# Kernel tuning notes

Measured on AMD Instinct MI355X. Metric: run time of the kernel, lower is better.

## Reference

```python
import jax, jax.numpy as jnp
import numpy as np

EPS = 1e-6

def _ln(x):
    m = jnp.mean(x, -1, keepdims=True)
    v = jnp.mean((x - m) ** 2, -1, keepdims=True)
    return (x - m) * jax.lax.rsqrt(v + EPS)

def _rms(x, w):
    return x * jax.lax.rsqrt(jnp.mean(x * x, -1, keepdims=True) + EPS) * w

def _rotate_half(x):
    xr = x.reshape(x.shape[:-1] + (-1, 2))
    return jnp.stack([-xr[..., 1], xr[..., 0]], axis=-1).reshape(x.shape)

def _rope(x, cos, sin):
    # x: [B,L,H,D]; cos/sin: [L,D] interleaved-duplicated per pair
    c = cos[None, :, None, :]
    s = sin[None, :, None, :]
    return x * c + _rotate_half(x) * s

def _modulate(x, shift, scale):
    return x * (1.0 + scale[:, None, :]) + shift[:, None, :]

def _gate(x, g):
    return x * g[:, None, :]

def setup_inputs() -> dict:
    key = jax.random.key(0)
    ks = jax.random.split(key, 20)
    B, LI, LT, D, NH, HD, M = 1, 2048, 256, 2048, 16, 128, 8192
    def n(k, shape, s=1.0):
        return jax.random.normal(k, shape, dtype=jnp.float32) * s
    theta = jax.random.uniform(ks[0], (LI, HD // 2), dtype=jnp.float32) * 6.2831853
    freqs_cos = jnp.repeat(jnp.cos(theta), 2, axis=-1)  # [LI, HD]
    freqs_sin = jnp.repeat(jnp.sin(theta), 2, axis=-1)
    inp = {
        'img': n(ks[1], (B, LI, D)),
        'txt': n(ks[2], (B, LT, D)),
        'vec': n(ks[3], (B, D)),
        'freqs_cos': freqs_cos,
        'freqs_sin': freqs_sin,
        'attn_mask': jnp.ones((B, LI + LT), dtype=bool),
        # img stream params
        'img_mod_w': n(ks[4], (D, 6 * D), 0.02), 'img_mod_b': jnp.zeros((6 * D,), jnp.float32),
        'img_qkv_w': n(ks[5], (D, 3 * D), 0.02),
        'img_qn_w': jnp.ones((HD,), jnp.float32), 'img_kn_w': jnp.ones((HD,), jnp.float32),
        'img_proj_w': n(ks[6], (D, D), 0.02),
        'img_fc1_w': n(ks[7], (D, M), 0.02), 'img_fc1_b': jnp.zeros((M,), jnp.float32),
        'img_fc2_w': n(ks[8], (M, D), 0.02), 'img_fc2_b': jnp.zeros((D,), jnp.float32),
        # txt stream params
        'txt_mod_w': n(ks[9], (D, 6 * D), 0.02), 'txt_mod_b': jnp.zeros((6 * D,), jnp.float32),
        'txt_qkv_w': n(ks[10], (D, 3 * D), 0.02),
        'txt_qn_w': jnp.ones((HD,), jnp.float32), 'txt_kn_w': jnp.ones((HD,), jnp.float32),
        'txt_proj_w': n(ks[11], (D, D), 0.02),
        'txt_fc1_w': n(ks[12], (D, M), 0.02), 'txt_fc1_b': jnp.zeros((M,), jnp.float32),
        'txt_fc2_w': n(ks[13], (M, D), 0.02), 'txt_fc2_b': jnp.zeros((D,), jnp.float32),
    }
    return inp

def reference(img, txt, vec, freqs_cos, freqs_sin, attn_mask,
              img_mod_w, img_mod_b, img_qkv_w, img_qn_w, img_kn_w, img_proj_w,
              img_fc1_w, img_fc1_b, img_fc2_w, img_fc2_b,
              txt_mod_w, txt_mod_b, txt_qkv_w, txt_qn_w, txt_kn_w, txt_proj_w,
              txt_fc1_w, txt_fc1_b, txt_fc2_w, txt_fc2_b):
    B, LI, D = img.shape
    LT = txt.shape[1]
    HD = img_qn_w.shape[0]
    NH = D // HD
    vec_s = jax.nn.silu(vec)
    im = vec_s @ img_mod_w + img_mod_b
    i_s1, i_sc1, i_g1, i_s2, i_sc2, i_g2 = jnp.split(im, 6, axis=-1)
    tm = vec_s @ txt_mod_w + txt_mod_b
    t_s1, t_sc1, t_g1, t_s2, t_sc2, t_g2 = jnp.split(tm, 6, axis=-1)
    # img pre-attention
    ix = _modulate(_ln(img), i_s1, i_sc1)
    iqkv = (ix @ img_qkv_w).reshape(B, LI, 3, NH, HD)
    iq = _rms(iqkv[:, :, 0], img_qn_w)
    ik = _rms(iqkv[:, :, 1], img_kn_w)
    iv = iqkv[:, :, 2]
    iq = _rope(iq, freqs_cos, freqs_sin)
    ik = _rope(ik, freqs_cos, freqs_sin)
    # txt pre-attention (no rope)
    tx = _modulate(_ln(txt), t_s1, t_sc1)
    tqkv = (tx @ txt_qkv_w).reshape(B, LT, 3, NH, HD)
    tq = _rms(tqkv[:, :, 0], txt_qn_w)
    tk = _rms(tqkv[:, :, 1], txt_kn_w)
    tv = tqkv[:, :, 2]
    # joint attention over concat(img, txt)
    q = jnp.concatenate([iq, tq], axis=1)  # [B,S,H,D]
    k = jnp.concatenate([ik, tk], axis=1)
    v = jnp.concatenate([iv, tv], axis=1)
    scores = jnp.einsum('bqhd,bkhd->bhqk', q, k) / jnp.sqrt(jnp.float32(HD))
    scores = jnp.where(attn_mask[:, None, None, :], scores, jnp.float32(-1e30))
    p = jax.nn.softmax(scores, axis=-1)
    attn = jnp.einsum('bhqk,bkhd->bqhd', p, v).reshape(B, LI + LT, D)
    img_attn, txt_attn = attn[:, :LI], attn[:, LI:]
    # img residual branches
    img = img + _gate(img_attn @ img_proj_w, i_g1)
    h = _modulate(_ln(img), i_s2, i_sc2)
    h = jax.nn.gelu(h @ img_fc1_w + img_fc1_b, approximate=True) @ img_fc2_w + img_fc2_b
    img = img + _gate(h, i_g2)
    # txt residual branches
    txt = txt + _gate(txt_attn @ txt_proj_w, t_g1)
    h = _modulate(_ln(txt), t_s2, t_sc2)
    h = jax.nn.gelu(h @ txt_fc1_w + txt_fc1_b, approximate=True) @ txt_fc2_w + txt_fc2_b
    txt = txt + _gate(h, t_g2)
    return (img, txt)
```

## Files before the change

### kernel.cpp

```cpp
#include <hip/hip_runtime.h>
#include <hip/hip_bf16.h>
#include <cstdint>
#include <cstddef>

typedef __bf16 bf16x8 __attribute__((ext_vector_type(8)));
typedef float  f32x4  __attribute__((ext_vector_type(4)));
typedef __hip_bfloat16 hbf16;

#define DEVI static __device__ __forceinline__

DEVI unsigned short f2bf_bits(float x){
  hbf16 h = __float2bfloat16(x);
  return *reinterpret_cast<unsigned short*>(&h);
}
DEVI float gelu_tanh(float x){
  float u = x*(1.0f + 0.044715f*x*x);
  float t = exp2f(-2.3022119f*u);
  return x/(1.0f+t);
}

typedef __attribute__((address_space(1))) const unsigned int* gas_p;
typedef __attribute__((address_space(3))) unsigned int* las_p;
DEVI void gload16(const void* g, void* l){
  __builtin_amdgcn_global_load_lds((gas_p)g, (las_p)l, 16, 0, 0);
}


__global__ void silu_k(const float* __restrict__ v, float* __restrict__ o, int n){
  int i = blockIdx.x*blockDim.x + threadIdx.x;
  if (i < n){ float x = v[i]; o[i] = x/(1.0f+__expf(-x)); }
}

__global__ __launch_bounds__(256) void mod_part_k(const float* __restrict__ vs,
                                                  const float* __restrict__ W,
                                                  float* __restrict__ part){
  int j  = blockIdx.x*1024 + threadIdx.x*4;
  int i0 = blockIdx.y*256;
  float4 acc = {0.f,0.f,0.f,0.f};
  for (int i=0;i<256;i++){
    float s = vs[i0+i];
    float4 w = *(const float4*)(W + (size_t)(i0+i)*12288 + j);
    acc.x += s*w.x; acc.y += s*w.y; acc.z += s*w.z; acc.w += s*w.w;
  }
  *(float4*)(part + (size_t)blockIdx.y*12288 + j) = acc;
}

__global__ __launch_bounds__(256) void mod_red_k(const float* __restrict__ part,
                                                 const float* __restrict__ b,
                                                 float* __restrict__ out){
  int j = blockIdx.x*1024 + threadIdx.x*4;
  float4 acc = *(const float4*)(b + j);
  #pragma unroll
  for (int y=0;y<8;y++){
    float4 p = *(const float4*)(part + (size_t)y*12288 + j);
    acc.x += p.x; acc.y += p.y; acc.z += p.z; acc.w += p.w;
  }
  *(float4*)(out + j) = acc;
}

__global__ __launch_bounds__(256) void ln_mod_k(
    const float* __restrict__ Xi, const float* __restrict__ Xt,
    const float* __restrict__ sh_i, const float* __restrict__ sc_i,
    const float* __restrict__ sh_t, const float* __restrict__ sc_t,
    hbf16* __restrict__ Yi, hbf16* __restrict__ Yt){
  __shared__ float red[8];
  const int row = blockIdx.x, tid = threadIdx.x;
  const float* X; const float* sh; const float* sc; hbf16* Y; int r;
  if (row < 2048){ X = Xi; sh = sh_i; sc = sc_i; Y = Yi; r = row; }
  else           { X = Xt; sh = sh_t; sc = sc_t; Y = Yt; r = row - 2048; }
  const float* x = X + (size_t)r*2048;
  float4 a = *(const float4*)(x + tid*8);
  float4 c = *(const float4*)(x + tid*8 + 4);
  float s  = a.x+a.y+a.z+a.w + c.x+c.y+c.z+c.w;
  float s2 = a.x*a.x+a.y*a.y+a.z*a.z+a.w*a.w + c.x*c.x+c.y*c.y+c.z*c.z+c.w*c.w;
  #pragma unroll
  for (int m=1;m<64;m<<=1){ s += __shfl_xor(s,m,64); s2 += __shfl_xor(s2,m,64); }
  if ((tid&63)==0){ red[tid>>6] = s; red[4+(tid>>6)] = s2; }
  __syncthreads();
  float S  = red[0]+red[1]+red[2]+red[3];
  float S2 = red[4]+red[5]+red[6]+red[7];
  float mean = S*(1.f/2048.f);
  float var  = S2*(1.f/2048.f) - mean*mean;
  float rs = rsqrtf(var + 1e-6f);
  float xv[8] = {a.x,a.y,a.z,a.w,c.x,c.y,c.z,c.w};
  #pragma unroll
  for (int j=0;j<8;j++){
    int n = tid*8 + j;
    float yv = (xv[j]-mean)*rs*(1.f+sc[n]) + sh[n];
    Y[(size_t)r*2048 + n] = __float2bfloat16(yv);
  }
}

__global__ __launch_bounds__(256) void transp3_k(const float* __restrict__ W1,
                                                 hbf16* __restrict__ Wt1,
                                                 const float* __restrict__ W2,
                                                 hbf16* __restrict__ Wt2,
                                                 int K, int N){
  const float* W = blockIdx.z ? W2 : W1;
  hbf16* Wt = blockIdx.z ? Wt2 : Wt1;
  __shared__ float tile[128][68];
  const int n0 = blockIdx.x*64, k0 = blockIdx.y*128;
  const int tid = threadIdx.x;
  #pragma unroll
  for (int i=0;i<8;i++){
    int c = i*256 + tid;
    int k = c>>4, nq = c&15;
    float4 v = *(const float4*)(W + (size_t)(k0+k)*N + n0 + nq*4);
    *(float4*)&tile[k][nq*4] = v;
  }
  __syncthreads();
  const int n = tid>>2, kseg = tid&3;
  unsigned short buf[32];
  #pragma unroll
  for (int j=0;j<32;j++) buf[j] = f2bf_bits(tile[kseg*32+j][n]);
  hbf16* dst = Wt + (size_t)(n0+n)*K + k0 + kseg*32;
  *(uint4*)(dst)      = *(const uint4*)&buf[0];
  *(uint4*)(dst + 8)  = *(const uint4*)&buf[8];
  *(uint4*)(dst + 16) = *(const uint4*)&buf[16];
  *(uint4*)(dst + 24) = *(const uint4*)&buf[24];
}

__global__ __launch_bounds__(256) void vtransp_k(const hbf16* __restrict__ V,
                                                 hbf16* __restrict__ Vt){
  __shared__ unsigned short tile[64][72];
  const int t0 = blockIdx.x*64, d0 = blockIdx.y*64;
  const int tid = threadIdx.x;
  #pragma unroll
  for (int i=0;i<2;i++){
    int c = i*256 + tid, row = c>>3, jj = c&7;
    uint4 v = *(const uint4*)(V + (size_t)(t0+row)*2048 + d0 + jj*8);
    *(uint4*)&tile[row][jj*8] = v;
  }
  __syncthreads();
  const int d = tid>>2, seg = tid&3;
  unsigned short buf[16];
  #pragma unroll
  for (int j=0;j<16;j++) buf[j] = tile[seg*16+j][d];
  *(uint4*)(Vt + (size_t)(d0+d)*2304 + t0 + seg*16)     = *(const uint4*)&buf[0];
  *(uint4*)(Vt + (size_t)(d0+d)*2304 + t0 + seg*16 + 8) = *(const uint4*)&buf[8];
}

__global__ __launch_bounds__(256) void rmsrope_k(
    const hbf16* __restrict__ iqkv, const hbf16* __restrict__ tqkv,
    const float* __restrict__ iqn, const float* __restrict__ ikn,
    const float* __restrict__ tqn, const float* __restrict__ tkn,
    const float* __restrict__ fcos, const float* __restrict__ fsin,
    hbf16* __restrict__ qb, hbf16* __restrict__ kb, hbf16* __restrict__ vb){
  const int t = blockIdx.x, tid = threadIdx.x;
  const bool isimg = (t < 2048);
  const hbf16* base = isimg ? (iqkv + (size_t)t*6144) : (tqkv + (size_t)(t-2048)*6144);
  const float* qw = isimg ? iqn : tqn;
  const float* kw = isimg ? ikn : tkn;
  const int head = tid>>4, li = tid&15, d0 = li*8;
  const int col = head*128 + d0;
  #pragma unroll
  for (int which=0; which<2; ++which){
    const hbf16* src = base + which*2048 + col;
    const float* w   = which ? kw : qw;
    bf16x8 raw = *(const bf16x8*)src;
    float xv[8];
    #pragma unroll
    for (int j=0;j<8;j++) xv[j] = (float)raw[j];
    float ss = 0.f;
    #pragma unroll
    for (int j=0;j<8;j++) ss += xv[j]*xv[j];
    #pragma unroll
    for (int m=1;m<16;m<<=1) ss += __shfl_xor(ss,m,16);
    float rs = rsqrtf(ss*(1.f/128.f) + 1e-6f);
    if (which==0) rs *= 0.12751745f;
    float y[8];
    #pragma unroll
    for (int j=0;j<8;j++) y[j] = xv[j]*rs*w[d0+j];
    if (isimg){
      const float* cp = fcos + (size_t)t*128 + d0;
      const float* sp = fsin + (size_t)t*128 + d0;
      float z[8];
      #pragma unroll
      for (int j=0;j<8;j+=2){
        z[j]   = y[j]*cp[j]     - y[j+1]*sp[j];
        z[j+1] = y[j+1]*cp[j+1] + y[j]*sp[j+1];
      }
      #pragma unroll
      for (int j=0;j<8;j++) y[j] = z[j];
    }
    hbf16* dst = (which ? kb : qb) + (size_t)t*2048 + col;
    #pragma unroll
    for (int j=0;j<8;j++) dst[j] = __float2bfloat16(y[j]);
  }
  {
    const int idx = tid*8;
    *(uint4*)(vb + (size_t)t*2048 + idx) = *(const uint4*)(base + 4096 + idx);
  }
}

template<int EPI>
__global__ __launch_bounds__(256,4) void gemm_k(
    const hbf16* __restrict__ A1, const hbf16* __restrict__ B1,
    float* __restrict__ Cf1, hbf16* __restrict__ Cb1,
    const float* __restrict__ bias1, const float* __restrict__ gate1,
    const float* __restrict__ res1,
    const hbf16* __restrict__ A2, const hbf16* __restrict__ B2,
    float* __restrict__ Cf2, hbf16* __restrict__ Cb2,
    const float* __restrict__ bias2, const float* __restrict__ gate2,
    const float* __restrict__ res2,
    int nbx, int nby1, int nby2, int N, int K)
{
  __shared__ unsigned short As[128*64];
  __shared__ unsigned short Bs[128*64];
  const int tid = threadIdx.x;
  const int wv = tid>>6, ln = tid&63;
  const int nwg = nbx*(nby1+nby2), q = nwg>>3;
  const int w  = blockIdx.x;
  const int w2 = (w&7)*q + (w>>3);
  int n0, m0;
  const hbf16* A; const hbf16* Bt; float* Cf; hbf16* Cb;
  const float* bias; const float* gate; const float* res;
  if (w2 < nbx*nby1){
    n0 = (w2/nby1)*128; m0 = (w2%nby1)*128;
    A=A1; Bt=B1; Cf=Cf1; Cb=Cb1; bias=bias1; gate=gate1; res=res1;
  } else {
    int w3 = w2 - nbx*nby1;
    n0 = (w3/nby2)*128; m0 = (w3%nby2)*128;
    A=A2; Bt=B2; Cf=Cf2; Cb=Cb2; bias=bias2; gate=gate2; res=res2;
  }
  const int wm = (wv>>1)*64, wn = (wv&1)*64;
  f32x4 acc[4][4];
  #pragma unroll
  for (int i=0;i<4;i++)
    #pragma unroll
    for (int j=0;j<4;j++) acc[i][j] = (f32x4){0.f,0.f,0.f,0.f};

  const int lrow = ln>>3;
  const int jsrc = (ln&7) ^ lrow;
  const int NT = K>>6;

  for (int kt=0; kt<NT; ++kt){
    const int kk = kt<<6;
    #pragma unroll
    for (int j=0;j<4;j++){
      int row = wv*32 + j*8 + lrow;
      gload16(A  + (size_t)(m0+row)*K + kk + jsrc*8, &As[(wv*4+j)*512]);
      gload16(Bt + (size_t)(n0+row)*K + kk + jsrc*8, &Bs[(wv*4+j)*512]);
    }
    __syncthreads();
    #pragma unroll
    for (int ks=0; ks<2; ++ks){
      bf16x8 af[4], bfv[4];
      #pragma unroll
      for (int qq=0;qq<4;qq++){
        int row = wm + qq*16 + (ln&15);
        int jj  = ks*4 + (ln>>4);
        af[qq] = *(const bf16x8*)&As[row*64 + ((jj^(row&7))<<3)];
      }
      #pragma unroll
      for (int qq=0;qq<4;qq++){
        int row = wn + qq*16 + (ln&15);
        int jj  = ks*4 + (ln>>4);
        bfv[qq] = *(const bf16x8*)&Bs[row*64 + ((jj^(row&7))<<3)];
      }
      #pragma unroll
      for (int i=0;i<4;i++)
        #pragma unroll
        for (int j=0;j<4;j++)
          acc[i][j] = __builtin_amdgcn_mfma_f32_16x16x32_bf16(af[i], bfv[j], acc[i][j], 0,0,0);
    }
    __syncthreads();
  }
  #pragma unroll
  for (int i=0;i<4;i++){
    int mbase = m0 + wm + i*16 + ((ln>>4)<<2);
    #pragma unroll
    for (int j=0;j<4;j++){
      int n = n0 + wn + j*16 + (ln&15);
      #pragma unroll
      for (int r=0;r<4;r++){
        size_t idx = (size_t)(mbase+r)*N + n;
        float v = acc[i][j][r];
        if constexpr (EPI==0){ Cf[idx] = v; }
        else if constexpr (EPI==1){ Cb[idx] = __float2bfloat16(gelu_tanh(v + bias[n])); }
        else if constexpr (EPI==2){ Cf[idx] = res[idx] + gate[n]*v; }
        else if constexpr (EPI==3){ Cf[idx] = res[idx] + gate[n]*(v + bias[n]); }
        else { Cb[idx] = __float2bfloat16(v); }
      }
    }
  }
}

__global__ __launch_bounds__(512,4) void attn_k(
    const hbf16* __restrict__ Qg, const hbf16* __restrict__ Kg,
    const hbf16* __restrict__ Vtg, float* __restrict__ sop01,
    float* __restrict__ sop23, float* __restrict__ mlp)
{
  const int w = blockIdx.x;
  const int h = w & 15, quarter = (w>>4)&3, q0 = (w>>6)*128;
  const int tid = threadIdx.x, wv = tid>>6, ln = tid&63;
  __shared__ unsigned short Ks[2][64*128];
  __shared__ unsigned short Vs[2][128*64];
  __shared__ unsigned short Ps[8][16*64];

  bf16x8 qf[4];
  {
    const hbf16* qrow = Qg + (size_t)(q0 + wv*16 + (ln&15))*2048 + h*128 + (ln>>4)*8;
    #pragma unroll
    for (int ks=0;ks<4;ks++) qf[ks] = *(const bf16x8*)(qrow + ks*32);
  }

  f32x4 so[8];
  #pragma unroll
  for (int i=0;i<8;i++) so[i] = (f32x4){0.f,0.f,0.f,0.f};
  float m_run[4] = {-3e38f,-3e38f,-3e38f,-3e38f};
  float l_run[4] = {0.f,0.f,0.f,0.f};

  auto stage = [&](int buf, int kt){
    const int k0 = kt*64;
    #pragma unroll
    for (int i=0;i<2;i++){
      int c = i*512 + tid;
      int row = c>>4, jj = c&15;
      int js = jj ^ (row&7);
      gload16(Kg + (size_t)(k0+row)*2048 + h*128 + js*8, &Ks[buf][(i*512 + wv*64)*8]);
    }
    #pragma unroll
    for (int i=0;i<2;i++){
      int c = i*512 + tid;
      int row = c>>3, jj = c&7;
      int js = jj ^ (row&7);
      gload16(Vtg + (size_t)(h*128+row)*2304 + k0 + js*8, &Vs[buf][(i*512 + wv*64)*8]);
    }
  };

  const int t0 = quarter*9;
  stage(0, t0);
  __syncthreads();

  for (int it=0; it<9; ++it){
    const int cur = it&1;
    if (it+1 < 9) stage(cur^1, t0+it+1);

    f32x4 s[4];
    #pragma unroll
    for (int nb=0;nb<4;nb++) s[nb] = (f32x4){0.f,0.f,0.f,0.f};
    __builtin_amdgcn_s_setprio(1);
    #pragma unroll
    for (int ks=0;ks<4;ks++){
      #pragma unroll
      for (int nb=0;nb<4;nb++){
        int rk = nb*16 + (ln&15);
        int jq = ks*4 + (ln>>4);
        bf16x8 bk = *(const bf16x8*)&Ks[cur][rk*128 + ((jq^(rk&7))<<3)];
        s[nb] = __builtin_amdgcn_mfma_f32_16x16x32_bf16(qf[ks], bk, s[nb], 0,0,0);
      }
    }
    __builtin_amdgcn_s_setprio(0);

    float scl[4];
    #pragma unroll
    for (int r=0;r<4;r++){
      float m1 = fmaxf(fmaxf(s[0][r], s[1][r]), fmaxf(s[2][r], s[3][r]));
      #pragma unroll
      for (int msk=1; msk<16; msk<<=1) m1 = fmaxf(m1, __shfl_xor(m1, msk, 64));
      float mn = fmaxf(m_run[r], m1);
      scl[r] = exp2f(m_run[r] - mn);
      m_run[r] = mn;
    }
    #pragma unroll
    for (int nb=0;nb<4;nb++)
      #pragma unroll
      for (int r=0;r<4;r++)
        s[nb][r] = exp2f(s[nb][r] - m_run[r]);
    #pragma unroll
    for (int r=0;r<4;r++){
      float sm = s[0][r]+s[1][r]+s[2][r]+s[3][r];
      #pragma unroll
      for (int msk=1; msk<16; msk<<=1) sm += __shfl_xor(sm, msk, 64);
      l_run[r] = l_run[r]*scl[r] + sm;
    }
    #pragma unroll
    for (int nb2=0;nb2<8;nb2++)
      #pragma unroll
      for (int r=0;r<4;r++) so[nb2][r] *= scl[r];

    #pragma unroll
    for (int nb=0;nb<4;nb++)
      #pragma unroll
      for (int r=0;r<4;r++){
        int m = ((ln>>4)<<2) + r;
        int n = nb*16 + (ln&15);
        Ps[wv][m*64 + (((n>>3)^(m&7))<<3) + (n&7)] = f2bf_bits(s[nb][r]);
      }

    __builtin_amdgcn_s_setprio(1);
    #pragma unroll
    for (int ks=0;ks<2;ks++){
      int mrow = ln&15;
      bf16x8 pa = *(const bf16x8*)&Ps[wv][mrow*64 + (((ks*4+(ln>>4))^(mrow&7))<<3)];
      #pragma unroll
      for (int nb2=0;nb2<8;nb2++){
        int rv = nb2*16 + (ln&15);
        int jv = ks*4 + (ln>>4);
        bf16x8 bv = *(const bf16x8*)&Vs[cur][rv*64 + ((jv^(rv&7))<<3)];
        so[nb2] = __builtin_amdgcn_mfma_f32_16x16x32_bf16(pa, bv, so[nb2], 0,0,0);
      }
    }
    __builtin_amdgcn_s_setprio(0);
    __syncthreads();
  }

  float* sbase = (quarter < 2 ? sop01 + (size_t)quarter*2304*2048
                              : sop23 + (size_t)(quarter-2)*2304*2048);
  #pragma unroll
  for (int r=0;r<4;r++){
    int m = q0 + wv*16 + ((ln>>4)<<2) + r;
    #pragma unroll
    for (int nb2=0;nb2<8;nb2++){
      int d = h*128 + nb2*16 + (ln&15);
      sbase[(size_t)m*2048 + d] = so[nb2][r];
    }
  }
  if ((ln&15)==0){
    #pragma unroll
    for (int r=0;r<4;r++){
      int m = q0 + wv*16 + ((ln>>4)<<2) + r;
      float* p = mlp + ((size_t)(quarter*2304 + m)*16 + h)*2;
      p[0] = m_run[r]; p[1] = l_run[r];
    }
  }
}

__global__ __launch_bounds__(256) void amerge_k(const float* __restrict__ sop01,
                                                const float* __restrict__ sop23,
                                                const float* __restrict__ mlp,
                                                hbf16* __restrict__ Og){
  const int q = blockIdx.x, tid = threadIdx.x;
  const int d0 = tid*8, h = tid>>4;
  float mv[4], lv[4];
  float m = -3e38f;
  #pragma unroll
  for (int h4=0;h4<4;h4++){
    const float* p = mlp + ((size_t)(h4*2304 + q)*16 + h)*2;
    mv[h4] = p[0]; lv[h4] = p[1];
    m = fmaxf(m, mv[h4]);
  }
  float wgt[4], den = 0.f;
  #pragma unroll
  for (int h4=0;h4<4;h4++){ wgt[h4] = exp2f(mv[h4]-m); den += wgt[h4]*lv[h4]; }
  float inv = 1.0f/den;
  float acc[8] = {0,0,0,0,0,0,0,0};
  #pragma unroll
  for (int h4=0;h4<4;h4++){
    const float* s = (h4<2 ? sop01 + (size_t)h4*2304*2048
                           : sop23 + (size_t)(h4-2)*2304*2048) + (size_t)q*2048 + d0;
    float4 a = *(const float4*)s, b = *(const float4*)(s+4);
    acc[0]+=wgt[h4]*a.x; acc[1]+=wgt[h4]*a.y; acc[2]+=wgt[h4]*a.z; acc[3]+=wgt[h4]*a.w;
    acc[4]+=wgt[h4]*b.x; acc[5]+=wgt[h4]*b.y; acc[6]+=wgt[h4]*b.z; acc[7]+=wgt[h4]*b.w;
  }
  hbf16* o = Og + (size_t)q*2048 + d0;
  #pragma unroll
  for (int j=0;j<8;j++) o[j] = __float2bfloat16(acc[j]*inv);
}


extern "C" void kernel_launch(void* const* d_in, const int* in_sizes, int n_in,
                              void* d_out, int out_size, void* d_ws, size_t ws_size,
                              hipStream_t stream) {
  (void)in_sizes; (void)n_in; (void)out_size; (void)ws_size;
  const float* img   = (const float*)d_in[0];
  const float* txt   = (const float*)d_in[1];
  const float* vec   = (const float*)d_in[2];
  const float* fcos  = (const float*)d_in[3];
  const float* fsin  = (const float*)d_in[4];
  const float* img_mod_w = (const float*)d_in[6];
  const float* img_mod_b = (const float*)d_in[7];
  const float* img_qkv_w = (const float*)d_in[8];
  const float* img_qn_w  = (const float*)d_in[9];
  const float* img_kn_w  = (const float*)d_in[10];
  const float* img_proj_w= (const float*)d_in[11];
  const float* img_fc1_w = (const float*)d_in[12];
  const float* img_fc1_b = (const float*)d_in[13];
  const float* img_fc2_w = (const float*)d_in[14];
  const float* img_fc2_b = (const float*)d_in[15];
  const float* txt_mod_w = (const float*)d_in[16];
  const float* txt_mod_b = (const float*)d_in[17];
  const float* txt_qkv_w = (const float*)d_in[18];
  const float* txt_qn_w  = (const float*)d_in[19];
  const float* txt_kn_w  = (const float*)d_in[20];
  const float* txt_proj_w= (const float*)d_in[21];
  const float* txt_fc1_w = (const float*)d_in[22];
  const float* txt_fc1_b = (const float*)d_in[23];
  const float* txt_fc2_w = (const float*)d_in[24];
  const float* txt_fc2_b = (const float*)d_in[25];

  float* out_img = (float*)d_out;
  float* out_txt = out_img + (size_t)2048*2048;

  char* ws = (char*)d_ws;
  size_t off = 0;
  auto alloc = [&](size_t bytes)->void*{
    void* p = ws + off; off += (bytes + 255) & ~(size_t)255; return p;
  };
  hbf16* wt1     = (hbf16*)alloc((size_t)16777216*2);
  hbf16* wt2     = (hbf16*)alloc((size_t)16777216*2);
  float* vs      = (float*)alloc(2048*4);
  float* im      = (float*)alloc(12288*4);
  float* tm      = (float*)alloc(12288*4);
  float* part    = (float*)alloc((size_t)2*8*12288*4);
  hbf16* ix      = (hbf16*)alloc((size_t)2048*2048*2);
  hbf16* tx      = (hbf16*)alloc((size_t)256*2048*2);
  hbf16* iqkvb   = (hbf16*)alloc((size_t)2048*6144*2);
  hbf16* tqkvb   = (hbf16*)alloc((size_t)256*6144*2);
  hbf16* qb      = (hbf16*)alloc((size_t)2304*2048*2);
  hbf16* kb      = (hbf16*)alloc((size_t)2304*2048*2);
  hbf16* vb      = (hbf16*)alloc((size_t)2304*2048*2);
  hbf16* vtg     = (hbf16*)alloc((size_t)2048*2304*2);
  hbf16* attnb   = (hbf16*)alloc((size_t)2304*2048*2);
  float* img_mid = (float*)alloc((size_t)2048*2048*4);
  float* txt_mid = (float*)alloc((size_t)256*2048*4);
  hbf16* ix2     = (hbf16*)alloc((size_t)2048*2048*2);
  hbf16* tx2     = (hbf16*)alloc((size_t)256*2048*2);
  hbf16* h1i     = (hbf16*)alloc((size_t)2048*8192*2);
  hbf16* h1t     = (hbf16*)alloc((size_t)256*8192*2);
  float* mlp     = (float*)alloc((size_t)4*2304*16*2*4);
  float* sop01 = (float*)ix;
  float* sop23 = (float*)img_mid;

  silu_k<<<8,256,0,stream>>>(vec, vs, 2048);
  mod_part_k<<<dim3(12,8),256,0,stream>>>(vs, img_mod_w, part);
  mod_part_k<<<dim3(12,8),256,0,stream>>>(vs, txt_mod_w, part + (size_t)8*12288);
  mod_red_k<<<12,256,0,stream>>>(part, img_mod_b, im);
  mod_red_k<<<12,256,0,stream>>>(part + (size_t)8*12288, txt_mod_b, tm);

  ln_mod_k<<<2304,256,0,stream>>>(img, txt, im+0, im+2048, tm+0, tm+2048, ix, tx);

  transp3_k<<<dim3(96,16,2),256,0,stream>>>(img_qkv_w, wt1, txt_qkv_w, wt2, 2048, 6144);
  gemm_k<4><<<864,256,0,stream>>>(ix, wt1, nullptr, iqkvb, nullptr, nullptr, nullptr,
                                  tx, wt2, nullptr, tqkvb, nullptr, nullptr, nullptr,
                                  48, 16, 2, 6144, 2048);

  rmsrope_k<<<2304,256,0,stream>>>(iqkvb, tqkvb, img_qn_w, img_kn_w, txt_qn_w, txt_kn_w,
                                   fcos, fsin, qb, kb, vb);
  vtransp_k<<<dim3(36,32),256,0,stream>>>(vb, vtg);

  attn_k<<<1152,512,0,stream>>>(qb, kb, vtg, sop01, sop23, mlp);
  amerge_k<<<2304,256,0,stream>>>(sop01, sop23, mlp, attnb);

  transp3_k<<<dim3(32,16,2),256,0,stream>>>(img_proj_w, wt1, txt_proj_w, wt2, 2048, 2048);
  gemm_k<2><<<288,256,0,stream>>>(attnb, wt1, img_mid, nullptr, nullptr, im+4096, img,
                                  attnb + (size_t)2048*2048, wt2, txt_mid, nullptr, nullptr, tm+4096, txt,
                                  16, 16, 2, 2048, 2048);

  ln_mod_k<<<2304,256,0,stream>>>(img_mid, txt_mid, im+6144, im+8192, tm+6144, tm+8192, ix2, tx2);

  transp3_k<<<dim3(128,16,2),256,0,stream>>>(img_fc1_w, wt1, txt_fc1_w, wt2, 2048, 8192);
  gemm_k<1><<<1152,256,0,stream>>>(ix2, wt1, nullptr, h1i, img_fc1_b, nullptr, nullptr,
                                   tx2, wt2, nullptr, h1t, txt_fc1_b, nullptr, nullptr,
                                   64, 16, 2, 8192, 2048);

  transp3_k<<<dim3(32,64,2),256,0,stream>>>(img_fc2_w, wt1, txt_fc2_w, wt2, 8192, 2048);
  gemm_k<3><<<288,256,0,stream>>>(h1i, wt1, out_img, nullptr, img_fc2_b, im+10240, img_mid,
                                  h1t, wt2, out_txt, nullptr, txt_fc2_b, tm+10240, txt_mid,
                                  16, 16, 2, 2048, 8192);
}
```

Measured before the change: 709.4 us.

## Use 256x128 GEMM tiles for QKV and FC1, split modulation reduction finer

Adds a new GEMM kernel with 256-row by 128-column tiles, so each wave computes an 8x4 grid of MFMA blocks. It replaces the previous GEMM for the QKV and FC1 projections, halving the workgroup count and raising operand reuse per LDS load. The modulation matvec is also split into 32 K-chunks instead of 8 to spread the weight read over more blocks. The trade-offs are higher register use from 128 accumulators per lane, a single-buffered LDS loop, and fewer workgroups to hide latency.

After: 833.2 us. +17.5%, slower.

```diff
diff --git a/kernel.cpp b/kernel.cpp
--- a/kernel.cpp
+++ b/kernel.cpp
@@ -35,9 +35,9 @@
                                                   const float* __restrict__ W,
                                                   float* __restrict__ part){
   int j  = blockIdx.x*1024 + threadIdx.x*4;
-  int i0 = blockIdx.y*256;
+  int i0 = blockIdx.y*64;
   float4 acc = {0.f,0.f,0.f,0.f};
-  for (int i=0;i<256;i++){
+  for (int i=0;i<64;i++){
     float s = vs[i0+i];
     float4 w = *(const float4*)(W + (size_t)(i0+i)*12288 + j);
     acc.x += s*w.x; acc.y += s*w.y; acc.z += s*w.z; acc.w += s*w.w;
@@ -51,7 +51,7 @@
   int j = blockIdx.x*1024 + threadIdx.x*4;
   float4 acc = *(const float4*)(b + j);
   #pragma unroll
-  for (int y=0;y<8;y++){
+  for (int y=0;y<32;y++){
     float4 p = *(const float4*)(part + (size_t)y*12288 + j);
     acc.x += p.x; acc.y += p.y; acc.z += p.z; acc.w += p.w;
   }
@@ -286,6 +286,96 @@
   }
 }
 
+template<int EPI>
+__global__ __launch_bounds__(256) void gemm256m_k(
+    const hbf16* __restrict__ A1, const hbf16* __restrict__ B1,
+    float* __restrict__ Cf1, hbf16* __restrict__ Cb1,
+    const float* __restrict__ bias1,
+    const hbf16* __restrict__ A2, const hbf16* __restrict__ B2,
+    float* __restrict__ Cf2, hbf16* __restrict__ Cb2,
+    const float* __restrict__ bias2,
+    int nbx, int nby1, int nby2, int N, int K)
+{
+  __shared__ unsigned short As[256*64];
+  __shared__ unsigned short Bs[128*64];
+  const int tid = threadIdx.x;
+  const int wv = tid>>6, ln = tid&63;
+  const int nwg = nbx*(nby1+nby2), q = nwg>>3;
+  const int w  = blockIdx.x;
+  const int w2 = (w&7)*q + (w>>3);
+  int n0, m0;
+  const hbf16* A; const hbf16* Bt; float* Cf; hbf16* Cb; const float* bias;
+  if (w2 < nbx*nby1){
+    n0 = (w2/nby1)*128; m0 = (w2%nby1)*256;
+    A=A1; Bt=B1; Cf=Cf1; Cb=Cb1; bias=bias1;
+  } else {
+    int w3 = w2 - nbx*nby1;
+    n0 = (w3/nby2)*128; m0 = (w3%nby2)*256;
+    A=A2; Bt=B2; Cf=Cf2; Cb=Cb2; bias=bias2;
+  }
+  const int wm = wv>>1, wn = wv&1;
+  const int lm = ln&15, lk = ln>>4;
+  f32x4 acc[8][4];
+  #pragma unroll
+  for (int i=0;i<8;i++)
+    #pragma unroll
+    for (int j=0;j<4;j++) acc[i][j] = (f32x4){0.f,0.f,0.f,0.f};
+
+  const int lrow = ln>>3;
+  const int jsrc = (ln&7) ^ lrow;
+  const int NT = K>>6;
+
+  for (int kt=0; kt<NT; ++kt){
+    const int kk = kt<<6;
+    #pragma unroll
+    for (int i=0;i<8;i++){
+      int row = i*32 + wv*8 + lrow;
+      gload16(A + (size_t)(m0+row)*K + kk + jsrc*8, &As[(i*32 + wv*8)*64]);
+    }
+    #pragma unroll
+    for (int i=0;i<4;i++){
+      int row = i*32 + wv*8 + lrow;
+      gload16(Bt + (size_t)(n0+row)*K + kk + jsrc*8, &Bs[(i*32 + wv*8)*64]);
+    }
+    __syncthreads();
+    #pragma unroll
+    for (int ks=0; ks<2; ++ks){
+      const int cs = (((ks*4+lk) ^ (lm&7))<<3);
+      bf16x8 af[8], bfv[4];
+      #pragma unroll
+      for (int qq=0;qq<8;qq++)
+        af[qq] = *(const bf16x8*)&As[(wm*128 + qq*16 + lm)*64 + cs];
+      #pragma unroll
+      for (int p=0;p<4;p++)
+        bfv[p] = *(const bf16x8*)&Bs[(wn*64 + p*16 + lm)*64 + cs];
+      __builtin_amdgcn_s_setprio(1);
+      #pragma unroll
+      for (int qq=0;qq<8;qq++)
+        #pragma unroll
+        for (int p=0;p<4;p++)
+          acc[qq][p] = __builtin_amdgcn_mfma_f32_16x16x32_bf16(af[qq], bfv[p], acc[qq][p], 0,0,0);
+      __builtin_amdgcn_s_setprio(0);
+    }
+    __syncthreads();
+  }
+  #pragma unroll
+  for (int qq=0;qq<8;qq++){
+    int mbase = m0 + wm*128 + qq*16 + lk*4;
+    #pragma unroll
+    for (int p=0;p<4;p++){
+      int n = n0 + wn*64 + p*16 + lm;
+      #pragma unroll
+      for (int r=0;r<4;r++){
+        size_t idx = (size_t)(mbase+r)*N + n;
+        float v = acc[qq][p][r];
+        if constexpr (EPI==1){ Cb[idx] = __float2bfloat16(gelu_tanh(v + bias[n])); }
+        else if constexpr (EPI==4){ Cb[idx] = __float2bfloat16(v); }
+        else { Cf[idx] = v; }
+      }
+    }
+  }
+}
+
 __global__ __launch_bounds__(512,4) void attn_k(
     const hbf16* __restrict__ Qg, const hbf16* __restrict__ Kg,
     const hbf16* __restrict__ Vtg, float* __restrict__ sop01,
@@ -503,7 +593,7 @@
   float* vs      = (float*)alloc(2048*4);
   float* im      = (float*)alloc(12288*4);
   float* tm      = (float*)alloc(12288*4);
-  float* part    = (float*)alloc((size_t)2*8*12288*4);
+  float* part    = (float*)alloc((size_t)2*32*12288*4);
   hbf16* ix      = (hbf16*)alloc((size_t)2048*2048*2);
   hbf16* tx      = (hbf16*)alloc((size_t)256*2048*2);
   hbf16* iqkvb   = (hbf16*)alloc((size_t)2048*6144*2);
@@ -524,17 +614,17 @@
   float* sop23 = (float*)img_mid;
 
   silu_k<<<8,256,0,stream>>>(vec, vs, 2048);
-  mod_part_k<<<dim3(12,8),256,0,stream>>>(vs, img_mod_w, part);
-  mod_part_k<<<dim3(12,8),256,0,stream>>>(vs, txt_mod_w, part + (size_t)8*12288);
+  mod_part_k<<<dim3(12,32),256,0,stream>>>(vs, img_mod_w, part);
+  mod_part_k<<<dim3(12,32),256,0,stream>>>(vs, txt_mod_w, part + (size_t)32*12288);
   mod_red_k<<<12,256,0,stream>>>(part, img_mod_b, im);
-  mod_red_k<<<12,256,0,stream>>>(part + (size_t)8*12288, txt_mod_b, tm);
+  mod_red_k<<<12,256,0,stream>>>(part + (size_t)32*12288, txt_mod_b, tm);
 
   ln_mod_k<<<2304,256,0,stream>>>(img, txt, im+0, im+2048, tm+0, tm+2048, ix, tx);
 
   transp3_k<<<dim3(96,16,2),256,0,stream>>>(img_qkv_w, wt1, txt_qkv_w, wt2, 2048, 6144);
-  gemm_k<4><<<864,256,0,stream>>>(ix, wt1, nullptr, iqkvb, nullptr, nullptr, nullptr,
-                                  tx, wt2, nullptr, tqkvb, nullptr, nullptr, nullptr,
-                                  48, 16, 2, 6144, 2048);
+  gemm256m_k<4><<<432,256,0,stream>>>(ix, wt1, nullptr, iqkvb, nullptr,
+                                      tx, wt2, nullptr, tqkvb, nullptr,
+                                      48, 8, 1, 6144, 2048);
 
   rmsrope_k<<<2304,256,0,stream>>>(iqkvb, tqkvb, img_qn_w, img_kn_w, txt_qn_w, txt_kn_w,
                                    fcos, fsin, qb, kb, vb);
@@ -551,9 +641,9 @@
   ln_mod_k<<<2304,256,0,stream>>>(img_mid, txt_mid, im+6144, im+8192, tm+6144, tm+8192, ix2, tx2);
 
   transp3_k<<<dim3(128,16,2),256,0,stream>>>(img_fc1_w, wt1, txt_fc1_w, wt2, 2048, 8192);
-  gemm_k<1><<<1152,256,0,stream>>>(ix2, wt1, nullptr, h1i, img_fc1_b, nullptr, nullptr,
-                                   tx2, wt2, nullptr, h1t, txt_fc1_b, nullptr, nullptr,
-                                   64, 16, 2, 8192, 2048);
+  gemm256m_k<1><<<576,256,0,stream>>>(ix2, wt1, nullptr, h1i, img_fc1_b,
+                                      tx2, wt2, nullptr, h1t, txt_fc1_b,
+                                      64, 8, 1, 8192, 2048);
 
   transp3_k<<<dim3(32,64,2),256,0,stream>>>(img_fc2_w, wt1, txt_fc2_w, wt2, 8192, 2048);
   gemm_k<3><<<288,256,0,stream>>>(h1i, wt1, out_img, nullptr, img_fc2_b, im+10240, img_mid,
```
